# Kernel tuning notes

Measured on AMD Instinct MI355X. Metric: run time of the kernel, lower is better.

## Reference

```python
import jax, jax.numpy as jnp
import numpy as np

DIM = 512
NUM_HEADS = 8
HEAD_DIM = DIM // NUM_HEADS
SCALE = HEAD_DIM ** -0.5
B, N, K_HOPS = 16, 1024, 5


def setup_inputs() -> dict:
    key = jax.random.key(0)
    ks = jax.random.split(key, 7)
    x = jax.random.normal(ks[0], (B, N, DIM), jnp.float32)
    Hstack = jax.random.uniform(ks[1], (K_HOPS, N, N), jnp.float32)
    hop_logits_attn = jax.random.normal(ks[2], (NUM_HEADS, K_HOPS), jnp.float32)
    rel_alpha = jax.random.normal(ks[3], (NUM_HEADS,), jnp.float32)
    Wqkv = jax.random.normal(ks[4], (3 * DIM, DIM), jnp.float32) * 0.02
    Wproj = jax.random.normal(ks[5], (DIM, DIM), jnp.float32) * 0.02
    bproj = jax.random.normal(ks[6], (DIM,), jnp.float32) * 0.02
    return {"x": x, "Hstack": Hstack, "hop_logits_attn": hop_logits_attn,
            "rel_alpha": rel_alpha, "Wqkv": Wqkv, "Wproj": Wproj, "bproj": bproj}


def reference(x, Hstack, hop_logits_attn, rel_alpha, Wqkv, Wproj, bproj):
    bs, n_tok, c_dim = x.shape
    # qkv projection: [B,N,3C] -> [3,B,H,N,hd]
    qkv = (x @ Wqkv.T).reshape(bs, n_tok, 3, NUM_HEADS, c_dim // NUM_HEADS)
    qkv = qkv.transpose(2, 0, 3, 1, 4)
    q, k, v = qkv[0], qkv[1], qkv[2]
    logits = jnp.einsum('bhnd,bhmd->bhnm', q, k) * SCALE  # [B,H,N,N]
    # hop-distance bias: per-head softmax mixture over K hop matrices
    w = jax.nn.softmax(hop_logits_attn, axis=-1)          # [H,K]
    B_head = jnp.einsum('hk,kij->hij', w, Hstack)          # [H,N,N]
    attn_bias = rel_alpha[:, None, None] * B_head          # [H,N,N]
    attn = jax.nn.softmax(logits + attn_bias[None], axis=-1)
    out = jnp.einsum('bhnm,bhmd->bhnd', attn, v)           # [B,H,N,hd]
    out = out.transpose(0, 2, 1, 3).reshape(bs, n_tok, c_dim)
    return out @ Wproj.T + bproj
```

## Files before the change

### kernel.cpp

```cpp
#include <hip/hip_runtime.h>
#include <hip/hip_bf16.h>
#include <hip/hip_fp16.h>
#include <stdint.h>

#define DIM   512
#define NH    8
#define HD    64
#define NB    16
#define NTOK  1024
#define KHOPS 5

typedef __attribute__((ext_vector_type(8))) short bf16x8;
typedef __attribute__((ext_vector_type(4))) float f32x4;

#define LOG2E 1.4426950408889634f

__device__ __forceinline__ unsigned short f32_to_bf16(float f) {
    unsigned int u = __builtin_bit_cast(unsigned int, f);
    unsigned int r = (u + 0x7FFFu + ((u >> 16) & 1u)) >> 16;
    return (unsigned short)r;
}

__device__ __forceinline__ float fast_exp2(float x) {
    return __builtin_amdgcn_exp2f(x);
}

#define AS1C(p) ((const __attribute__((address_space(1))) void*)(p))
#define AS3(p)  ((__attribute__((address_space(3))) void*)(p))

__global__ __launch_bounds__(256) void cvt_all(const float* __restrict__ x,
                                               const float* __restrict__ wq,
                                               const float* __restrict__ wp,
                                               unsigned short* __restrict__ xb,
                                               unsigned short* __restrict__ wqb,
                                               unsigned short* __restrict__ wpb) {
    int bid = blockIdx.x;
    const float* in; unsigned short* out; int i;
    if (bid < 8192)      { in = x;  out = xb;  i = bid * 256 + threadIdx.x; }
    else if (bid < 8960) { in = wq; out = wqb; i = (bid - 8192) * 256 + threadIdx.x; }
    else                 { in = wp; out = wpb; i = (bid - 8960) * 256 + threadIdx.x; }
    float4 v = reinterpret_cast<const float4*>(in)[i];
    ushort4 o;
    o.x = f32_to_bf16(v.x); o.y = f32_to_bf16(v.y);
    o.z = f32_to_bf16(v.z); o.w = f32_to_bf16(v.w);
    reinterpret_cast<ushort4*>(out)[i] = o;
}

__global__ __launch_bounds__(256) void bias_fused(const float* __restrict__ H,
                                                  const float* __restrict__ hop_logits,
                                                  const float* __restrict__ rel_alpha,
                                                  uint32_t* __restrict__ biast) {
    const int tid = threadIdx.x;
    const int jt = blockIdx.x, it = blockIdx.y;
    const int j0 = jt * 64, i0 = it * 64;
    float cf[NH][KHOPS];
#pragma unroll
    for (int h = 0; h < NH; ++h) {
        float m = -1e30f;
#pragma unroll
        for (int k = 0; k < KHOPS; ++k) m = fmaxf(m, hop_logits[h * KHOPS + k]);
        float s = 0.f;
#pragma unroll
        for (int k = 0; k < KHOPS; ++k) { cf[h][k] = fast_exp2((hop_logits[h * KHOPS + k] - m) * LOG2E); s += cf[h][k]; }
        float ra = rel_alpha[h] * LOG2E / s;
#pragma unroll
        for (int k = 0; k < KHOPS; ++k) cf[h][k] *= ra;
    }
    const int r = tid >> 2, c0 = (tid & 3) * 16;
    float hv[KHOPS][16];
#pragma unroll
    for (int k = 0; k < KHOPS; ++k) {
        const float4* src = reinterpret_cast<const float4*>(
            H + (size_t)k * 1048576 + (size_t)(i0 + r) * 1024 + j0 + c0);
#pragma unroll
        for (int q = 0; q < 4; ++q) {
            float4 v = src[q];
            hv[k][q * 4 + 0] = v.x; hv[k][q * 4 + 1] = v.y;
            hv[k][q * 4 + 2] = v.z; hv[k][q * 4 + 3] = v.w;
        }
    }
    for (int h = 0; h < NH; ++h) {
        uint32_t buf[8];
#pragma unroll
        for (int q = 0; q < 4; ++q) {
            float a0 = 0.f, a1 = 0.f, a2 = 0.f, a3 = 0.f;
#pragma unroll
            for (int k = 0; k < KHOPS; ++k) {
                a0 += cf[h][k] * hv[k][q * 4 + 0];
                a1 += cf[h][k] * hv[k][q * 4 + 1];
                a2 += cf[h][k] * hv[k][q * 4 + 2];
                a3 += cf[h][k] * hv[k][q * 4 + 3];
            }
            buf[q * 2 + 0] = __builtin_bit_cast(uint32_t, __floats2half2_rn(a0, a1));
            buf[q * 2 + 1] = __builtin_bit_cast(uint32_t, __floats2half2_rn(a2, a3));
        }
        uint32_t* dst = biast + ((size_t)h * 1024 + i0 + r) * 512 + ((j0 + c0) >> 1);
        uint4 w0; w0.x = buf[0]; w0.y = buf[1]; w0.z = buf[2]; w0.w = buf[3];
        uint4 w1; w1.x = buf[4]; w1.y = buf[5]; w1.z = buf[6]; w1.w = buf[7];
        reinterpret_cast<uint4*>(dst)[0] = w0;
        reinterpret_cast<uint4*>(dst)[1] = w1;
    }
}

__global__ __launch_bounds__(256) void gemm_qkv(const unsigned short* __restrict__ A,
                                                const unsigned short* __restrict__ Bw,
                                                unsigned short* __restrict__ qkv,
                                                unsigned short* __restrict__ vt) {
    __shared__ unsigned short As[128 * 32];
    __shared__ unsigned short Bs[128 * 32];
    const int tid  = threadIdx.x;
    const int lane = tid & 63;
    const int w    = tid >> 6;
    const int wr   = (w >> 1) * 64, wc = (w & 1) * 64;
    const int l15  = lane & 15, quad = lane >> 4;
    const int bid  = blockIdx.x;
    const int xcd  = bid & 7, slot = bid >> 3;
    const int m0   = (xcd * 16 + (slot & 15)) * 128;
    const int n0   = (slot >> 4) * 128;
    const int K = 512, Nn = 1536;

    f32x4 acc[4][4];
#pragma unroll
    for (int i = 0; i < 4; ++i)
#pragma unroll
        for (int j = 0; j < 4; ++j) { acc[i][j][0] = 0.f; acc[i][j][1] = 0.f; acc[i][j][2] = 0.f; acc[i][j][3] = 0.f; }

    for (int k0 = 0; k0 < K; k0 += 32) {
        __syncthreads();
#pragma unroll
        for (int t = 0; t < 2; ++t) {
            int c = t * 256 + w * 64 + lane;
            int r = c >> 2, kh = c & 3;
            const unsigned short* ga = A  + (size_t)(m0 + r) * K + k0 + kh * 8;
            const unsigned short* gb = Bw + (size_t)(n0 + r) * K + k0 + kh * 8;
            __builtin_amdgcn_global_load_lds(AS1C(ga), AS3(&As[(t * 256 + w * 64) * 8]), 16, 0, 0);
            __builtin_amdgcn_global_load_lds(AS1C(gb), AS3(&Bs[(t * 256 + w * 64) * 8]), 16, 0, 0);
        }
        __syncthreads();
        bf16x8 af[4], bfr[4];
#pragma unroll
        for (int rt = 0; rt < 4; ++rt)
            af[rt] = *reinterpret_cast<const bf16x8*>(&As[(wr + rt * 16 + l15) * 32 + quad * 8]);
#pragma unroll
        for (int ct = 0; ct < 4; ++ct)
            bfr[ct] = *reinterpret_cast<const bf16x8*>(&Bs[(wc + ct * 16 + l15) * 32 + quad * 8]);
#pragma unroll
        for (int rt = 0; rt < 4; ++rt)
#pragma unroll
            for (int ct = 0; ct < 4; ++ct)
                acc[rt][ct] = __builtin_amdgcn_mfma_f32_16x16x32_bf16(af[rt], bfr[ct], acc[rt][ct], 0, 0, 0);
    }

    if (n0 < 1024) {
#pragma unroll
        for (int rt = 0; rt < 4; ++rt)
#pragma unroll
            for (int ct = 0; ct < 4; ++ct)
#pragma unroll
                for (int reg = 0; reg < 4; ++reg) {
                    int row = m0 + wr + rt * 16 + quad * 4 + reg;
                    int col = n0 + wc + ct * 16 + l15;
                    qkv[(size_t)row * Nn + col] = f32_to_bf16(acc[rt][ct][reg]);
                }
    } else {
        const int b = m0 >> 10;
#pragma unroll
        for (int ct = 0; ct < 4; ++ct) {
            int c = n0 - 1024 + wc + ct * 16 + l15;
            unsigned short* vrow = vt + ((size_t)(b * 8) * 64 + c) * 1024;
#pragma unroll
            for (int rt = 0; rt < 4; ++rt) {
                int trow = (m0 & 1023) + wr + rt * 16 + quad * 4;
                ushort4 pk;
                pk.x = f32_to_bf16(acc[rt][ct][0]);
                pk.y = f32_to_bf16(acc[rt][ct][1]);
                pk.z = f32_to_bf16(acc[rt][ct][2]);
                pk.w = f32_to_bf16(acc[rt][ct][3]);
                *reinterpret_cast<ushort4*>(vrow + trow) = pk;
            }
        }
    }
}

__global__ __launch_bounds__(256) void gemm_proj(const unsigned short* __restrict__ A,
                                                 const unsigned short* __restrict__ Bw,
                                                 float* __restrict__ C,
                                                 const float* __restrict__ cbias) {
    __shared__ unsigned short As[128 * 32];
    __shared__ unsigned short Bs[128 * 32];
    const int tid  = threadIdx.x;
    const int lane = tid & 63;
    const int w    = tid >> 6;
    const int wr   = (w >> 1) * 64, wc = (w & 1) * 64;
    const int l15  = lane & 15, quad = lane >> 4;
    const int bid  = blockIdx.x;
    const int xcd  = bid & 7, slot = bid >> 3;
    const int m0   = (xcd * 16 + (slot & 15)) * 128;
    const int n0   = (slot >> 4) * 128;
    const int K = 512, Nn = 512;

    f32x4 acc[4][4];
#pragma unroll
    for (int i = 0; i < 4; ++i)
#pragma unroll
        for (int j = 0; j < 4; ++j) { acc[i][j][0] = 0.f; acc[i][j][1] = 0.f; acc[i][j][2] = 0.f; acc[i][j][3] = 0.f; }

    for (int k0 = 0; k0 < K; k0 += 32) {
        __syncthreads();
#pragma unroll
        for (int t = 0; t < 2; ++t) {
            int c = t * 256 + w * 64 + lane;
            int r = c >> 2, kh = c & 3;
            const unsigned short* ga = A  + (size_t)(m0 + r) * K + k0 + kh * 8;
            const unsigned short* gb = Bw + (size_t)(n0 + r) * K + k0 + kh * 8;
            __builtin_amdgcn_global_load_lds(AS1C(ga), AS3(&As[(t * 256 + w * 64) * 8]), 16, 0, 0);
            __builtin_amdgcn_global_load_lds(AS1C(gb), AS3(&Bs[(t * 256 + w * 64) * 8]), 16, 0, 0);
        }
        __syncthreads();
        bf16x8 af[4], bfr[4];
#pragma unroll
        for (int rt = 0; rt < 4; ++rt)
            af[rt] = *reinterpret_cast<const bf16x8*>(&As[(wr + rt * 16 + l15) * 32 + quad * 8]);
#pragma unroll
        for (int ct = 0; ct < 4; ++ct)
            bfr[ct] = *reinterpret_cast<const bf16x8*>(&Bs[(wc + ct * 16 + l15) * 32 + quad * 8]);
#pragma unroll
        for (int rt = 0; rt < 4; ++rt)
#pragma unroll
            for (int ct = 0; ct < 4; ++ct)
                acc[rt][ct] = __builtin_amdgcn_mfma_f32_16x16x32_bf16(af[rt], bfr[ct], acc[rt][ct], 0, 0, 0);
    }

#pragma unroll
    for (int ct = 0; ct < 4; ++ct) {
        int col = n0 + wc + ct * 16 + l15;
        float bv = cbias[col];
#pragma unroll
        for (int rt = 0; rt < 4; ++rt)
#pragma unroll
            for (int reg = 0; reg < 4; ++reg) {
                int row = m0 + wr + rt * 16 + quad * 4 + reg;
                C[(size_t)row * Nn + col] = acc[rt][ct][reg] + bv;
            }
    }
}

__global__ __launch_bounds__(256, 3) void flash_attn(const unsigned short* __restrict__ qkv,
                                                     const unsigned short* __restrict__ vt,
                                                     const uint32_t* __restrict__ biast,
                                                     unsigned short* __restrict__ aout) {
    __shared__ unsigned short Kb[2][64 * 64];
    __shared__ unsigned short Vb[2][64 * 64];
    __shared__ __align__(16) unsigned short Ps[4 * 32 * 72];
    const int tid  = threadIdx.x;
    const int lane = tid & 63, w = tid >> 6;
    const int l15  = lane & 15, quad = lane >> 4;
    const int h = blockIdx.x, qt = blockIdx.y, b = blockIdx.z;
    const int i0 = qt * 128 + w * 32;
    const float kscale = 0.125f * LOG2E;
    const int l7 = l15 & 7;

    bf16x8 qf[2][2];
#pragma unroll
    for (int rt = 0; rt < 2; ++rt)
#pragma unroll
        for (int ks = 0; ks < 2; ++ks)
            qf[rt][ks] = *reinterpret_cast<const bf16x8*>(
                qkv + (size_t)(b * 1024 + i0 + rt * 16 + l15) * 1536 + h * 64 + ks * 32 + quad * 8);

    f32x4 o[2][4];
    f32x4 lacc[2];
#pragma unroll
    for (int rt = 0; rt < 2; ++rt) {
#pragma unroll
        for (int nt = 0; nt < 4; ++nt) { o[rt][nt][0] = 0.f; o[rt][nt][1] = 0.f; o[rt][nt][2] = 0.f; o[rt][nt][3] = 0.f; }
        lacc[rt][0] = 0.f; lacc[rt][1] = 0.f; lacc[rt][2] = 0.f; lacc[rt][3] = 0.f;
    }

    bf16x8 ones;
#pragma unroll
    for (int e = 0; e < 8; ++e) ones[e] = (short)0x3F80;

    const int srow = lane >> 3;
    const int gch  = (lane & 7) ^ srow;
    const unsigned short* kgbase = qkv + (size_t)b * 1024 * 1536 + 512 + h * 64 + gch * 8;
    const unsigned short* vgbase = vt + (size_t)((b * 8 + h) * 64) * 1024 + gch * 8;
    const uint32_t* bb = biast + ((size_t)h * 1024 + i0) * 512;
    unsigned short* ps = &Ps[w * 32 * 72];

#pragma unroll
    for (int t = 0; t < 2; ++t) {
        int rl = w * 16 + t * 8 + srow;
        __builtin_amdgcn_global_load_lds(AS1C(kgbase + (size_t)rl * 1536),
                                         AS3(&Kb[0][(w * 16 + t * 8) * 64]), 16, 0, 0);
        __builtin_amdgcn_global_load_lds(AS1C(vgbase + (size_t)rl * 1024),
                                         AS3(&Vb[0][(w * 16 + t * 8) * 64]), 16, 0, 0);
    }

#pragma unroll 2
    for (int it = 0; it < 16; ++it) {
        const int cur = it & 1, nxt = cur ^ 1;
        const int j0 = it * 64;
        __syncthreads();

        if (it < 15) {
            const int j0n = j0 + 64;
#pragma unroll
            for (int t = 0; t < 2; ++t) {
                int rl = w * 16 + t * 8 + srow;
                __builtin_amdgcn_global_load_lds(AS1C(kgbase + (size_t)(j0n + rl) * 1536),
                                                 AS3(&Kb[nxt][(w * 16 + t * 8) * 64]), 16, 0, 0);
                __builtin_amdgcn_global_load_lds(AS1C(vgbase + (size_t)rl * 1024 + j0n),
                                                 AS3(&Vb[nxt][(w * 16 + t * 8) * 64]), 16, 0, 0);
            }
        }

        uint2 bl[2][4];
#pragma unroll
        for (int rt = 0; rt < 2; ++rt)
#pragma unroll
            for (int jt = 0; jt < 4; ++jt)
                bl[rt][jt] = *reinterpret_cast<const uint2*>(
                    bb + (size_t)(rt * 16 + l15) * 512 + (j0 >> 1) + jt * 8 + quad * 2);

        f32x4 s[2][4];
#pragma unroll
        for (int rt = 0; rt < 2; ++rt)
#pragma unroll
            for (int jt = 0; jt < 4; ++jt) { s[rt][jt][0] = 0.f; s[rt][jt][1] = 0.f; s[rt][jt][2] = 0.f; s[rt][jt][3] = 0.f; }
#pragma unroll
        for (int ks = 0; ks < 2; ++ks) {
            bf16x8 kf[4];
#pragma unroll
            for (int jt = 0; jt < 4; ++jt)
                kf[jt] = *reinterpret_cast<const bf16x8*>(
                    &Kb[cur][(jt * 16 + l15) * 64 + (((ks * 4 + quad) ^ l7) * 8)]);
#pragma unroll
            for (int rt = 0; rt < 2; ++rt)
#pragma unroll
                for (int jt = 0; jt < 4; ++jt)
                    s[rt][jt] = __builtin_amdgcn_mfma_f32_16x16x32_bf16(kf[jt], qf[rt][ks], s[rt][jt], 0, 0, 0);
        }

#pragma unroll
        for (int rt = 0; rt < 2; ++rt)
#pragma unroll
            for (int jt = 0; jt < 4; ++jt) {
                float2 f0 = __half22float2(__builtin_bit_cast(__half2, bl[rt][jt].x));
                float2 f1 = __half22float2(__builtin_bit_cast(__half2, bl[rt][jt].y));
                float p0 = fast_exp2(__builtin_fmaf(s[rt][jt][0], kscale, f0.x));
                float p1 = fast_exp2(__builtin_fmaf(s[rt][jt][1], kscale, f0.y));
                float p2 = fast_exp2(__builtin_fmaf(s[rt][jt][2], kscale, f1.x));
                float p3 = fast_exp2(__builtin_fmaf(s[rt][jt][3], kscale, f1.y));
                uint32_t u0 = (uint32_t)f32_to_bf16(p0) | ((uint32_t)f32_to_bf16(p1) << 16);
                uint32_t u1 = (uint32_t)f32_to_bf16(p2) | ((uint32_t)f32_to_bf16(p3) << 16);
                uint2 pk; pk.x = u0; pk.y = u1;
                *reinterpret_cast<uint2*>(ps + (rt * 16 + l15) * 72 + jt * 16 + quad * 4) = pk;
            }

#pragma unroll
        for (int ks = 0; ks < 2; ++ks) {
            bf16x8 pf[2], vf[4];
#pragma unroll
            for (int rt = 0; rt < 2; ++rt)
                pf[rt] = *reinterpret_cast<const bf16x8*>(ps + (rt * 16 + l15) * 72 + ks * 32 + quad * 8);
#pragma unroll
            for (int nt = 0; nt < 4; ++nt)
                vf[nt] = *reinterpret_cast<const bf16x8*>(
                    &Vb[cur][(nt * 16 + l15) * 64 + (((ks * 4 + quad) ^ l7) * 8)]);
#pragma unroll
            for (int rt = 0; rt < 2; ++rt) {
#pragma unroll
                for (int nt = 0; nt < 4; ++nt)
                    o[rt][nt] = __builtin_amdgcn_mfma_f32_16x16x32_bf16(pf[rt], vf[nt], o[rt][nt], 0, 0, 0);
                lacc[rt] = __builtin_amdgcn_mfma_f32_16x16x32_bf16(pf[rt], ones, lacc[rt], 0, 0, 0);
            }
        }
    }

#pragma unroll
    for (int rt = 0; rt < 2; ++rt) {
        float inv[4];
#pragma unroll
        for (int reg = 0; reg < 4; ++reg) inv[reg] = 1.f / lacc[rt][reg];
#pragma unroll
        for (int nt = 0; nt < 4; ++nt)
#pragma unroll
            for (int reg = 0; reg < 4; ++reg) {
                int row = b * 1024 + i0 + rt * 16 + quad * 4 + reg;
                int col = h * 64 + nt * 16 + l15;
                aout[(size_t)row * 512 + col] = f32_to_bf16(o[rt][nt][reg] * inv[reg]);
            }
    }
}

extern "C" void kernel_launch(void* const* d_in, const int* in_sizes, int n_in,
                              void* d_out, int out_size, void* d_ws, size_t ws_size,
                              hipStream_t stream) {
    const float* x          = (const float*)d_in[0];
    const float* Hstack     = (const float*)d_in[1];
    const float* hop_logits = (const float*)d_in[2];
    const float* rel_alpha  = (const float*)d_in[3];
    const float* Wqkv       = (const float*)d_in[4];
    const float* Wproj      = (const float*)d_in[5];
    const float* bproj      = (const float*)d_in[6];
    float* out = (float*)d_out;

    char* ws = (char*)d_ws;
    unsigned short* xb    = (unsigned short*)(ws);
    unsigned short* wqb   = (unsigned short*)(ws + 16777216);
    unsigned short* wpb   = (unsigned short*)(ws + 18350080);
    unsigned short* qkvb  = (unsigned short*)(ws + 18874368);
    unsigned short* vtb   = (unsigned short*)(ws + 69206016);
    uint32_t*       biast = (uint32_t*)(ws + 85983232);
    unsigned short* aoutb = (unsigned short*)(ws + 102760448);

    cvt_all<<<9216, 256, 0, stream>>>(x, Wqkv, Wproj, xb, wqb, wpb);

    bias_fused<<<dim3(16, 16), 256, 0, stream>>>(Hstack, hop_logits, rel_alpha, biast);

    gemm_qkv<<<1536, 256, 0, stream>>>(xb, wqb, qkvb, vtb);

    flash_attn<<<dim3(8, 8, 16), 256, 0, stream>>>(qkvb, vtb, biast, aoutb);

    gemm_proj<<<512, 256, 0, stream>>>(aoutb, wpb, out, bproj);
}
```

Baseline: 264.0 us.

## Widen GEMM K-tile to 64 with XOR-swizzled LDS and vectorized epilogues; fuse prep kernels

The QKV and projection GEMMs now stage 64-wide K slices in LDS using an XOR swizzle on 16-byte chunks, which halves the number of barrier pairs and avoids LDS bank conflicts on the fragment reads. For the Q/K output and the projection, operand order in the MFMA is swapped so each lane holds four consecutive columns, allowing vectorized 8-byte and 16-byte stores instead of scalar stores. The bf16 conversion kernel and the bias-building kernel are merged into a single launch to save one launch and let them overlap. LDS per block doubles, which may reduce occupancy.

```diff
diff --git a/kernel.cpp b/kernel.cpp
--- a/kernel.cpp
+++ b/kernel.cpp
@@ -28,30 +28,32 @@
 #define AS1C(p) ((const __attribute__((address_space(1))) void*)(p))
 #define AS3(p)  ((__attribute__((address_space(3))) void*)(p))
 
-__global__ __launch_bounds__(256) void cvt_all(const float* __restrict__ x,
-                                               const float* __restrict__ wq,
-                                               const float* __restrict__ wp,
-                                               unsigned short* __restrict__ xb,
-                                               unsigned short* __restrict__ wqb,
-                                               unsigned short* __restrict__ wpb) {
-    int bid = blockIdx.x;
-    const float* in; unsigned short* out; int i;
-    if (bid < 8192)      { in = x;  out = xb;  i = bid * 256 + threadIdx.x; }
-    else if (bid < 8960) { in = wq; out = wqb; i = (bid - 8192) * 256 + threadIdx.x; }
-    else                 { in = wp; out = wpb; i = (bid - 8960) * 256 + threadIdx.x; }
-    float4 v = reinterpret_cast<const float4*>(in)[i];
-    ushort4 o;
-    o.x = f32_to_bf16(v.x); o.y = f32_to_bf16(v.y);
-    o.z = f32_to_bf16(v.z); o.w = f32_to_bf16(v.w);
-    reinterpret_cast<ushort4*>(out)[i] = o;
-}
-
-__global__ __launch_bounds__(256) void bias_fused(const float* __restrict__ H,
-                                                  const float* __restrict__ hop_logits,
-                                                  const float* __restrict__ rel_alpha,
-                                                  uint32_t* __restrict__ biast) {
+__global__ __launch_bounds__(256) void cvt_bias(const float* __restrict__ x,
+                                                const float* __restrict__ wq,
+                                                const float* __restrict__ wp,
+                                                const float* __restrict__ H,
+                                                const float* __restrict__ hop_logits,
+                                                const float* __restrict__ rel_alpha,
+                                                unsigned short* __restrict__ xb,
+                                                unsigned short* __restrict__ wqb,
+                                                unsigned short* __restrict__ wpb,
+                                                uint32_t* __restrict__ biast) {
+    const int bid = blockIdx.x;
     const int tid = threadIdx.x;
-    const int jt = blockIdx.x, it = blockIdx.y;
+    if (bid < 9216) {
+        const float* in; unsigned short* out; int i;
+        if (bid < 8192)      { in = x;  out = xb;  i = bid * 256 + tid; }
+        else if (bid < 8960) { in = wq; out = wqb; i = (bid - 8192) * 256 + tid; }
+        else                 { in = wp; out = wpb; i = (bid - 8960) * 256 + tid; }
+        float4 v = reinterpret_cast<const float4*>(in)[i];
+        ushort4 o;
+        o.x = f32_to_bf16(v.x); o.y = f32_to_bf16(v.y);
+        o.z = f32_to_bf16(v.z); o.w = f32_to_bf16(v.w);
+        reinterpret_cast<ushort4*>(out)[i] = o;
+        return;
+    }
+    const int bb = bid - 9216;
+    const int jt = bb & 15, it = bb >> 4;
     const int j0 = jt * 64, i0 = it * 64;
     float cf[NH][KHOPS];
 #pragma unroll
@@ -106,8 +108,8 @@
                                                 const unsigned short* __restrict__ Bw,
                                                 unsigned short* __restrict__ qkv,
                                                 unsigned short* __restrict__ vt) {
-    __shared__ unsigned short As[128 * 32];
-    __shared__ unsigned short Bs[128 * 32];
+    __shared__ unsigned short As[128 * 64];
+    __shared__ unsigned short Bs[128 * 64];
     const int tid  = threadIdx.x;
     const int lane = tid & 63;
     const int w    = tid >> 6;
@@ -118,6 +120,7 @@
     const int m0   = (xcd * 16 + (slot & 15)) * 128;
     const int n0   = (slot >> 4) * 128;
     const int K = 512, Nn = 1536;
+    const int rA = l15 & 7;
 
     f32x4 acc[4][4];
 #pragma unroll
@@ -125,44 +128,84 @@
 #pragma unroll
         for (int j = 0; j < 4; ++j) { acc[i][j][0] = 0.f; acc[i][j][1] = 0.f; acc[i][j][2] = 0.f; acc[i][j][3] = 0.f; }
 
-    for (int k0 = 0; k0 < K; k0 += 32) {
-        __syncthreads();
-#pragma unroll
-        for (int t = 0; t < 2; ++t) {
-            int c = t * 256 + w * 64 + lane;
-            int r = c >> 2, kh = c & 3;
-            const unsigned short* ga = A  + (size_t)(m0 + r) * K + k0 + kh * 8;
-            const unsigned short* gb = Bw + (size_t)(n0 + r) * K + k0 + kh * 8;
-            __builtin_amdgcn_global_load_lds(AS1C(ga), AS3(&As[(t * 256 + w * 64) * 8]), 16, 0, 0);
-            __builtin_amdgcn_global_load_lds(AS1C(gb), AS3(&Bs[(t * 256 + w * 64) * 8]), 16, 0, 0);
-        }
-        __syncthreads();
-        bf16x8 af[4], bfr[4];
-#pragma unroll
-        for (int rt = 0; rt < 4; ++rt)
-            af[rt] = *reinterpret_cast<const bf16x8*>(&As[(wr + rt * 16 + l15) * 32 + quad * 8]);
-#pragma unroll
-        for (int ct = 0; ct < 4; ++ct)
-            bfr[ct] = *reinterpret_cast<const bf16x8*>(&Bs[(wc + ct * 16 + l15) * 32 + quad * 8]);
-#pragma unroll
-        for (int rt = 0; rt < 4; ++rt)
-#pragma unroll
-            for (int ct = 0; ct < 4; ++ct)
-                acc[rt][ct] = __builtin_amdgcn_mfma_f32_16x16x32_bf16(af[rt], bfr[ct], acc[rt][ct], 0, 0, 0);
-    }
-
     if (n0 < 1024) {
-#pragma unroll
-        for (int rt = 0; rt < 4; ++rt)
-#pragma unroll
-            for (int ct = 0; ct < 4; ++ct)
-#pragma unroll
-                for (int reg = 0; reg < 4; ++reg) {
-                    int row = m0 + wr + rt * 16 + quad * 4 + reg;
-                    int col = n0 + wc + ct * 16 + l15;
-                    qkv[(size_t)row * Nn + col] = f32_to_bf16(acc[rt][ct][reg]);
-                }
+        for (int k0 = 0; k0 < K; k0 += 64) {
+            __syncthreads();
+#pragma unroll
+            for (int t = 0; t < 4; ++t) {
+                int c = t * 256 + tid;
+                int row = c >> 3, ch = c & 7;
+                int gch = ch ^ (row & 7);
+                __builtin_amdgcn_global_load_lds(AS1C(A  + (size_t)(m0 + row) * K + k0 + gch * 8),
+                                                 AS3(&As[c * 8]), 16, 0, 0);
+                __builtin_amdgcn_global_load_lds(AS1C(Bw + (size_t)(n0 + row) * K + k0 + gch * 8),
+                                                 AS3(&Bs[c * 8]), 16, 0, 0);
+            }
+            __syncthreads();
+#pragma unroll
+            for (int ks = 0; ks < 2; ++ks) {
+                bf16x8 af[4], bfr[4];
+#pragma unroll
+                for (int rt = 0; rt < 4; ++rt)
+                    af[rt] = *reinterpret_cast<const bf16x8*>(
+                        &As[(wr + rt * 16 + l15) * 64 + (((ks * 4 + quad) ^ rA) * 8)]);
+#pragma unroll
+                for (int ct = 0; ct < 4; ++ct)
+                    bfr[ct] = *reinterpret_cast<const bf16x8*>(
+                        &Bs[(wc + ct * 16 + l15) * 64 + (((ks * 4 + quad) ^ rA) * 8)]);
+#pragma unroll
+                for (int ct = 0; ct < 4; ++ct)
+#pragma unroll
+                    for (int rt = 0; rt < 4; ++rt)
+                        acc[ct][rt] = __builtin_amdgcn_mfma_f32_16x16x32_bf16(bfr[ct], af[rt], acc[ct][rt], 0, 0, 0);
+            }
+        }
+#pragma unroll
+        for (int rt = 0; rt < 4; ++rt) {
+            int row = m0 + wr + rt * 16 + l15;
+#pragma unroll
+            for (int ct = 0; ct < 4; ++ct) {
+                int col = n0 + wc + ct * 16 + quad * 4;
+                ushort4 pk;
+                pk.x = f32_to_bf16(acc[ct][rt][0]);
+                pk.y = f32_to_bf16(acc[ct][rt][1]);
+                pk.z = f32_to_bf16(acc[ct][rt][2]);
+                pk.w = f32_to_bf16(acc[ct][rt][3]);
+                *reinterpret_cast<ushort4*>(qkv + (size_t)row * Nn + col) = pk;
+            }
+        }
     } else {
+        for (int k0 = 0; k0 < K; k0 += 64) {
+            __syncthreads();
+#pragma unroll
+            for (int t = 0; t < 4; ++t) {
+                int c = t * 256 + tid;
+                int row = c >> 3, ch = c & 7;
+                int gch = ch ^ (row & 7);
+                __builtin_amdgcn_global_load_lds(AS1C(A  + (size_t)(m0 + row) * K + k0 + gch * 8),
+                                                 AS3(&As[c * 8]), 16, 0, 0);
+                __builtin_amdgcn_global_load_lds(AS1C(Bw + (size_t)(n0 + row) * K + k0 + gch * 8),
+                                                 AS3(&Bs[c * 8]), 16, 0, 0);
+            }
+            __syncthreads();
+#pragma unroll
+            for (int ks = 0; ks < 2; ++ks) {
+                bf16x8 af[4], bfr[4];
+#pragma unroll
+                for (int rt = 0; rt < 4; ++rt)
+                    af[rt] = *reinterpret_cast<const bf16x8*>(
+                        &As[(wr + rt * 16 + l15) * 64 + (((ks * 4 + quad) ^ rA) * 8)]);
+#pragma unroll
+                for (int ct = 0; ct < 4; ++ct)
+                    bfr[ct] = *reinterpret_cast<const bf16x8*>(
+                        &Bs[(wc + ct * 16 + l15) * 64 + (((ks * 4 + quad) ^ rA) * 8)]);
+#pragma unroll
+                for (int rt = 0; rt < 4; ++rt)
+#pragma unroll
+                    for (int ct = 0; ct < 4; ++ct)
+                        acc[rt][ct] = __builtin_amdgcn_mfma_f32_16x16x32_bf16(af[rt], bfr[ct], acc[rt][ct], 0, 0, 0);
+            }
+        }
         const int b = m0 >> 10;
 #pragma unroll
         for (int ct = 0; ct < 4; ++ct) {
@@ -186,8 +229,8 @@
                                                  const unsigned short* __restrict__ Bw,
                                                  float* __restrict__ C,
                                                  const float* __restrict__ cbias) {
-    __shared__ unsigned short As[128 * 32];
-    __shared__ unsigned short Bs[128 * 32];
+    __shared__ unsigned short As[128 * 64];
+    __shared__ unsigned short Bs[128 * 64];
     const int tid  = threadIdx.x;
     const int lane = tid & 63;
     const int w    = tid >> 6;
@@ -198,6 +241,7 @@
     const int m0   = (xcd * 16 + (slot & 15)) * 128;
     const int n0   = (slot >> 4) * 128;
     const int K = 512, Nn = 512;
+    const int rA = l15 & 7;
 
     f32x4 acc[4][4];
 #pragma unroll
@@ -205,43 +249,52 @@
 #pragma unroll
         for (int j = 0; j < 4; ++j) { acc[i][j][0] = 0.f; acc[i][j][1] = 0.f; acc[i][j][2] = 0.f; acc[i][j][3] = 0.f; }
 
-    for (int k0 = 0; k0 < K; k0 += 32) {
+    for (int k0 = 0; k0 < K; k0 += 64) {
         __syncthreads();
 #pragma unroll
-        for (int t = 0; t < 2; ++t) {
-            int c = t * 256 + w * 64 + lane;
-            int r = c >> 2, kh = c & 3;
-            const unsigned short* ga = A  + (size_t)(m0 + r) * K + k0 + kh * 8;
-            const unsigned short* gb = Bw + (size_t)(n0 + r) * K + k0 + kh * 8;
-            __builtin_amdgcn_global_load_lds(AS1C(ga), AS3(&As[(t * 256 + w * 64) * 8]), 16, 0, 0);
-            __builtin_amdgcn_global_load_lds(AS1C(gb), AS3(&Bs[(t * 256 + w * 64) * 8]), 16, 0, 0);
+        for (int t = 0; t < 4; ++t) {
+            int c = t * 256 + tid;
+            int row = c >> 3, ch = c & 7;
+            int gch = ch ^ (row & 7);
+            __builtin_amdgcn_global_load_lds(AS1C(A  + (size_t)(m0 + row) * K + k0 + gch * 8),
+                                             AS3(&As[c * 8]), 16, 0, 0);
+            __builtin_amdgcn_global_load_lds(AS1C(Bw + (size_t)(n0 + row) * K + k0 + gch * 8),
+                                             AS3(&Bs[c * 8]), 16, 0, 0);
         }
         __syncthreads();
-        bf16x8 af[4], bfr[4];
-#pragma unroll
-        for (int rt = 0; rt < 4; ++rt)
-            af[rt] = *reinterpret_cast<const bf16x8*>(&As[(wr + rt * 16 + l15) * 32 + quad * 8]);
-#pragma unroll
-        for (int ct = 0; ct < 4; ++ct)
-            bfr[ct] = *reinterpret_cast<const bf16x8*>(&Bs[(wc + ct * 16 + l15) * 32 + quad * 8]);
-#pragma unroll
-        for (int rt = 0; rt < 4; ++rt)
+#pragma unroll
+        for (int ks = 0; ks < 2; ++ks) {
+            bf16x8 af[4], bfr[4];
+#pragma unroll
+            for (int rt = 0; rt < 4; ++rt)
+                af[rt] = *reinterpret_cast<const bf16x8*>(
+                    &As[(wr + rt * 16 + l15) * 64 + (((ks * 4 + quad) ^ rA) * 8)]);
 #pragma unroll
             for (int ct = 0; ct < 4; ++ct)
-                acc[rt][ct] = __builtin_amdgcn_mfma_f32_16x16x32_bf16(af[rt], bfr[ct], acc[rt][ct], 0, 0, 0);
+                bfr[ct] = *reinterpret_cast<const bf16x8*>(
+                    &Bs[(wc + ct * 16 + l15) * 64 + (((ks * 4 + quad) ^ rA) * 8)]);
+#pragma unroll
+            for (int ct = 0; ct < 4; ++ct)
+#pragma unroll
+                for (int rt = 0; rt < 4; ++rt)
+                    acc[ct][rt] = __builtin_amdgcn_mfma_f32_16x16x32_bf16(bfr[ct], af[rt], acc[ct][rt], 0, 0, 0);
+        }
     }
 
 #pragma unroll
     for (int ct = 0; ct < 4; ++ct) {
-        int col = n0 + wc + ct * 16 + l15;
-        float bv = cbias[col];
-#pragma unroll
-        for (int rt = 0; rt < 4; ++rt)
-#pragma unroll
-            for (int reg = 0; reg < 4; ++reg) {
-                int row = m0 + wr + rt * 16 + quad * 4 + reg;
-                C[(size_t)row * Nn + col] = acc[rt][ct][reg] + bv;
-            }
+        int col = n0 + wc + ct * 16 + quad * 4;
+        float4 bv = *reinterpret_cast<const float4*>(cbias + col);
+#pragma unroll
+        for (int rt = 0; rt < 4; ++rt) {
+            int row = m0 + wr + rt * 16 + l15;
+            float4 ov;
+            ov.x = acc[ct][rt][0] + bv.x;
+            ov.y = acc[ct][rt][1] + bv.y;
+            ov.z = acc[ct][rt][2] + bv.z;
+            ov.w = acc[ct][rt][3] + bv.w;
+            *reinterpret_cast<float4*>(C + (size_t)row * Nn + col) = ov;
+        }
     }
 }
 
@@ -415,9 +468,8 @@
     uint32_t*       biast = (uint32_t*)(ws + 85983232);
     unsigned short* aoutb = (unsigned short*)(ws + 102760448);
 
-    cvt_all<<<9216, 256, 0, stream>>>(x, Wqkv, Wproj, xb, wqb, wpb);
-
-    bias_fused<<<dim3(16, 16), 256, 0, stream>>>(Hstack, hop_logits, rel_alpha, biast);
+    cvt_bias<<<9472, 256, 0, stream>>>(x, Wqkv, Wproj, Hstack, hop_logits, rel_alpha,
+                                       xb, wqb, wpb, biast);
 
     gemm_qkv<<<1536, 256, 0, stream>>>(xb, wqb, qkvb, vtb);
 
```

Result: slower. 275.0 us (+4.2%).

## Double flash-attention query tile per wave to 64 rows with XOR-swizzled P buffer

Applied to the files above, without the earlier changes.

Each wave now handles 64 query rows instead of 32, so a block covers 256 queries and the grid halves along the query axis. Every K/V tile loaded into LDS is reused across twice as many queries, which cuts K/V global traffic and barrier count per unit of work. The P staging buffer drops its padding in favour of an XOR swizzle to avoid bank conflicts. The cost is higher register pressure (launch bounds lowered from 3 to 2 blocks per SM), more LDS per block, and fewer blocks in the grid, which may reduce occupancy and latency hiding.

```diff
diff --git a/kernel.cpp b/kernel.cpp
--- a/kernel.cpp
+++ b/kernel.cpp
@@ -245,33 +245,34 @@
     }
 }
 
-__global__ __launch_bounds__(256, 3) void flash_attn(const unsigned short* __restrict__ qkv,
+__global__ __launch_bounds__(256, 2) void flash_attn(const unsigned short* __restrict__ qkv,
                                                      const unsigned short* __restrict__ vt,
                                                      const uint32_t* __restrict__ biast,
                                                      unsigned short* __restrict__ aout) {
     __shared__ unsigned short Kb[2][64 * 64];
     __shared__ unsigned short Vb[2][64 * 64];
-    __shared__ __align__(16) unsigned short Ps[4 * 32 * 72];
+    __shared__ __align__(16) unsigned short Ps[4 * 64 * 64];
     const int tid  = threadIdx.x;
     const int lane = tid & 63, w = tid >> 6;
     const int l15  = lane & 15, quad = lane >> 4;
     const int h = blockIdx.x, qt = blockIdx.y, b = blockIdx.z;
-    const int i0 = qt * 128 + w * 32;
+    const int i0 = qt * 256 + w * 64;
     const float kscale = 0.125f * LOG2E;
     const int l7 = l15 & 7;
-
-    bf16x8 qf[2][2];
-#pragma unroll
-    for (int rt = 0; rt < 2; ++rt)
+    const int psw = l7 << 3;
+
+    bf16x8 qf[4][2];
+#pragma unroll
+    for (int rt = 0; rt < 4; ++rt)
 #pragma unroll
         for (int ks = 0; ks < 2; ++ks)
             qf[rt][ks] = *reinterpret_cast<const bf16x8*>(
                 qkv + (size_t)(b * 1024 + i0 + rt * 16 + l15) * 1536 + h * 64 + ks * 32 + quad * 8);
 
-    f32x4 o[2][4];
-    f32x4 lacc[2];
-#pragma unroll
-    for (int rt = 0; rt < 2; ++rt) {
+    f32x4 o[4][4];
+    f32x4 lacc[4];
+#pragma unroll
+    for (int rt = 0; rt < 4; ++rt) {
 #pragma unroll
         for (int nt = 0; nt < 4; ++nt) { o[rt][nt][0] = 0.f; o[rt][nt][1] = 0.f; o[rt][nt][2] = 0.f; o[rt][nt][3] = 0.f; }
         lacc[rt][0] = 0.f; lacc[rt][1] = 0.f; lacc[rt][2] = 0.f; lacc[rt][3] = 0.f;
@@ -286,7 +287,7 @@
     const unsigned short* kgbase = qkv + (size_t)b * 1024 * 1536 + 512 + h * 64 + gch * 8;
     const unsigned short* vgbase = vt + (size_t)((b * 8 + h) * 64) * 1024 + gch * 8;
     const uint32_t* bb = biast + ((size_t)h * 1024 + i0) * 512;
-    unsigned short* ps = &Ps[w * 32 * 72];
+    unsigned short* ps = &Ps[w * 64 * 64];
 
 #pragma unroll
     for (int t = 0; t < 2; ++t) {
@@ -315,71 +316,74 @@
             }
         }
 
-        uint2 bl[2][4];
-#pragma unroll
-        for (int rt = 0; rt < 2; ++rt)
+        uint2 bl[4][4];
+#pragma unroll
+        for (int rt = 0; rt < 4; ++rt)
 #pragma unroll
             for (int jt = 0; jt < 4; ++jt)
                 bl[rt][jt] = *reinterpret_cast<const uint2*>(
                     bb + (size_t)(rt * 16 + l15) * 512 + (j0 >> 1) + jt * 8 + quad * 2);
 
-        f32x4 s[2][4];
-#pragma unroll
-        for (int rt = 0; rt < 2; ++rt)
-#pragma unroll
-            for (int jt = 0; jt < 4; ++jt) { s[rt][jt][0] = 0.f; s[rt][jt][1] = 0.f; s[rt][jt][2] = 0.f; s[rt][jt][3] = 0.f; }
+#pragma unroll
+        for (int rp = 0; rp < 2; ++rp) {
+            f32x4 s[2][4];
+#pragma unroll
+            for (int r2 = 0; r2 < 2; ++r2)
+#pragma unroll
+                for (int jt = 0; jt < 4; ++jt) { s[r2][jt][0] = 0.f; s[r2][jt][1] = 0.f; s[r2][jt][2] = 0.f; s[r2][jt][3] = 0.f; }
+#pragma unroll
+            for (int ks = 0; ks < 2; ++ks) {
+                bf16x8 kf[4];
+#pragma unroll
+                for (int jt = 0; jt < 4; ++jt)
+                    kf[jt] = *reinterpret_cast<const bf16x8*>(
+                        &Kb[cur][(jt * 16 + l15) * 64 + (((ks * 4 + quad) ^ l7) * 8)]);
+#pragma unroll
+                for (int r2 = 0; r2 < 2; ++r2)
+#pragma unroll
+                    for (int jt = 0; jt < 4; ++jt)
+                        s[r2][jt] = __builtin_amdgcn_mfma_f32_16x16x32_bf16(kf[jt], qf[rp * 2 + r2][ks], s[r2][jt], 0, 0, 0);
+            }
+#pragma unroll
+            for (int r2 = 0; r2 < 2; ++r2)
+#pragma unroll
+                for (int jt = 0; jt < 4; ++jt) {
+                    const int rt = rp * 2 + r2;
+                    float2 f0 = __half22float2(__builtin_bit_cast(__half2, bl[rt][jt].x));
+                    float2 f1 = __half22float2(__builtin_bit_cast(__half2, bl[rt][jt].y));
+                    float p0 = fast_exp2(__builtin_fmaf(s[r2][jt][0], kscale, f0.x));
+                    float p1 = fast_exp2(__builtin_fmaf(s[r2][jt][1], kscale, f0.y));
+                    float p2 = fast_exp2(__builtin_fmaf(s[r2][jt][2], kscale, f1.x));
+                    float p3 = fast_exp2(__builtin_fmaf(s[r2][jt][3], kscale, f1.y));
+                    uint32_t u0 = (uint32_t)f32_to_bf16(p0) | ((uint32_t)f32_to_bf16(p1) << 16);
+                    uint32_t u1 = (uint32_t)f32_to_bf16(p2) | ((uint32_t)f32_to_bf16(p3) << 16);
+                    uint2 pk; pk.x = u0; pk.y = u1;
+                    *reinterpret_cast<uint2*>(
+                        ps + (((rt * 16 + l15) * 64 + jt * 16 + quad * 4) ^ psw)) = pk;
+                }
+        }
+
 #pragma unroll
         for (int ks = 0; ks < 2; ++ks) {
-            bf16x8 kf[4];
-#pragma unroll
-            for (int jt = 0; jt < 4; ++jt)
-                kf[jt] = *reinterpret_cast<const bf16x8*>(
-                    &Kb[cur][(jt * 16 + l15) * 64 + (((ks * 4 + quad) ^ l7) * 8)]);
-#pragma unroll
-            for (int rt = 0; rt < 2; ++rt)
-#pragma unroll
-                for (int jt = 0; jt < 4; ++jt)
-                    s[rt][jt] = __builtin_amdgcn_mfma_f32_16x16x32_bf16(kf[jt], qf[rt][ks], s[rt][jt], 0, 0, 0);
-        }
-
-#pragma unroll
-        for (int rt = 0; rt < 2; ++rt)
-#pragma unroll
-            for (int jt = 0; jt < 4; ++jt) {
-                float2 f0 = __half22float2(__builtin_bit_cast(__half2, bl[rt][jt].x));
-                float2 f1 = __half22float2(__builtin_bit_cast(__half2, bl[rt][jt].y));
-                float p0 = fast_exp2(__builtin_fmaf(s[rt][jt][0], kscale, f0.x));
-                float p1 = fast_exp2(__builtin_fmaf(s[rt][jt][1], kscale, f0.y));
-                float p2 = fast_exp2(__builtin_fmaf(s[rt][jt][2], kscale, f1.x));
-                float p3 = fast_exp2(__builtin_fmaf(s[rt][jt][3], kscale, f1.y));
-                uint32_t u0 = (uint32_t)f32_to_bf16(p0) | ((uint32_t)f32_to_bf16(p1) << 16);
-                uint32_t u1 = (uint32_t)f32_to_bf16(p2) | ((uint32_t)f32_to_bf16(p3) << 16);
-                uint2 pk; pk.x = u0; pk.y = u1;
-                *reinterpret_cast<uint2*>(ps + (rt * 16 + l15) * 72 + jt * 16 + quad * 4) = pk;
-            }
-
-#pragma unroll
-        for (int ks = 0; ks < 2; ++ks) {
-            bf16x8 pf[2], vf[4];
-#pragma unroll
-            for (int rt = 0; rt < 2; ++rt)
-                pf[rt] = *reinterpret_cast<const bf16x8*>(ps + (rt * 16 + l15) * 72 + ks * 32 + quad * 8);
+            bf16x8 vf[4];
 #pragma unroll
             for (int nt = 0; nt < 4; ++nt)
                 vf[nt] = *reinterpret_cast<const bf16x8*>(
                     &Vb[cur][(nt * 16 + l15) * 64 + (((ks * 4 + quad) ^ l7) * 8)]);
 #pragma unroll
-            for (int rt = 0; rt < 2; ++rt) {
+            for (int rt = 0; rt < 4; ++rt) {
+                bf16x8 pf = *reinterpret_cast<const bf16x8*>(
+                    ps + (((rt * 16 + l15) * 64 + ks * 32 + quad * 8) ^ psw));
 #pragma unroll
                 for (int nt = 0; nt < 4; ++nt)
-                    o[rt][nt] = __builtin_amdgcn_mfma_f32_16x16x32_bf16(pf[rt], vf[nt], o[rt][nt], 0, 0, 0);
-                lacc[rt] = __builtin_amdgcn_mfma_f32_16x16x32_bf16(pf[rt], ones, lacc[rt], 0, 0, 0);
-            }
-        }
-    }
-
-#pragma unroll
-    for (int rt = 0; rt < 2; ++rt) {
+                    o[rt][nt] = __builtin_amdgcn_mfma_f32_16x16x32_bf16(pf, vf[nt], o[rt][nt], 0, 0, 0);
+                lacc[rt] = __builtin_amdgcn_mfma_f32_16x16x32_bf16(pf, ones, lacc[rt], 0, 0, 0);
+            }
+        }
+    }
+
+#pragma unroll
+    for (int rt = 0; rt < 4; ++rt) {
         float inv[4];
 #pragma unroll
         for (int reg = 0; reg < 4; ++reg) inv[reg] = 1.f / lacc[rt][reg];
@@ -421,7 +425,7 @@
 
     gemm_qkv<<<1536, 256, 0, stream>>>(xb, wqb, qkvb, vtb);
 
-    flash_attn<<<dim3(8, 8, 16), 256, 0, stream>>>(qkvb, vtb, biast, aoutb);
+    flash_attn<<<dim3(8, 4, 16), 256, 0, stream>>>(qkvb, vtb, biast, aoutb);
 
     gemm_proj<<<512, 256, 0, stream>>>(aoutb, wpb, out, bproj);
 }
```

New measurement: 266.9 us. Within noise of the previous version (+1.1%).
